# Optimization experiments

Measured on AMD Instinct MI355X. Metric: run time of the kernel, lower is better.

Reference implementation:

```python
import jax, jax.numpy as jnp
import numpy as np

GS, SO = 5, 3  # KANLinear grid_size, spline_order (efficient-kan defaults)


def kan_linear(x, base_w, spline_w, spline_scaler):
    """efficient-kan KANLinear: silu(x)@Wb^T + Bspline(x) contracted with scaled spline weights."""
    g = jnp.arange(-SO, GS + SO + 1, dtype=x.dtype) * (2.0 / GS) - 1.0  # uniform grid, len 12
    xe = x[..., None]                                                    # (..., in, 1)
    bases = ((xe >= g[:-1]) & (xe < g[1:])).astype(x.dtype)              # (..., in, 11)
    for k in range(1, SO + 1):  # Cox-de Boor recursion -> (..., in, 8)
        bases = ((xe - g[:-(k + 1)]) / (g[k:-1] - g[:-(k + 1)])) * bases[..., :-1] \
              + ((g[k + 1:] - xe) / (g[k + 1:] - g[1:-k])) * bases[..., 1:]
    out = jax.nn.silu(x) @ base_w.T
    return out + jnp.einsum('...ik,oik->...o', bases, spline_w * spline_scaler[..., None])


def reference(hidden_states, in_bw, in_sw, in_sc, conv_w, conv_b, x_bw, x_sw, x_sc,
              dt_w, dt_bias, A_logs, Ds, out_bw, out_sw, out_sc):
    B, N, L, Dm = hidden_states.shape
    d_inner, _, d_conv = conv_w.shape
    K = dt_bias.shape[0]          # 4 scan directions
    d_state = A_logs.shape[1]
    dt_rank = dt_w.shape[1]

    xz = kan_linear(hidden_states, in_bw, in_sw, in_sc)          # (B,N,L,2*Di)
    x, z = jnp.split(xz, 2, axis=-1)

    # causal depthwise conv1d + SiLU (torch pads both sides then truncates to L == left-pad)
    xc = x.reshape(B * N, L, d_inner).transpose(0, 2, 1)          # (BN,Di,L)
    xc = jax.lax.conv_general_dilated(xc, conv_w, (1,), [(d_conv - 1, 0)],
                                      dimension_numbers=('NCH', 'OIH', 'NCH'),
                                      feature_group_count=d_inner)
    xc = jax.nn.silu(xc + conv_b[None, :, None])
    x = xc.transpose(0, 2, 1).reshape(B, N, L, d_inner)

    xs = jnp.concatenate([x, jnp.flip(x, axis=2)], axis=1)        # (B,4,L,Di): fwd + seq-reversed

    x_dbl = kan_linear(xs, x_bw, x_sw, x_sc)                      # (B,4,L,R+2S)
    dt, Bs, Cs = jnp.split(x_dbl, [dt_rank, dt_rank + d_state], axis=-1)
    dts = dt @ dt_w.T                                             # (B,4,L,Di)
    delta = jax.nn.softplus(dts + dt_bias[None, :, None, :])      # (B,4,L,Di)
    A = -jnp.exp(A_logs).reshape(K, d_inner, d_state)             # (4,Di,S)

    # selective scan over L (serial data-dependent linear recurrence)
    u_t = xs.transpose(2, 0, 1, 3)      # (L,B,4,Di)
    d_t = delta.transpose(2, 0, 1, 3)   # (L,B,4,Di)
    B_t = Bs.transpose(2, 0, 1, 3)      # (L,B,4,S)
    C_t = Cs.transpose(2, 0, 1, 3)      # (L,B,4,S)

    def step(h, inp):
        u_l, dl, b_l, c_l = inp
        h = h * jnp.exp(dl[..., None] * A) + (dl * u_l)[..., None] * b_l[:, :, None, :]
        return h, jnp.einsum('bkdn,bkn->bkd', h, c_l)

    h0 = jnp.zeros((B, K, d_inner, d_state), xs.dtype)
    _, ys = jax.lax.scan(step, h0, (u_t, d_t, B_t, C_t))          # ys: (L,B,4,Di)

    y = ys.transpose(1, 2, 0, 3) + xs * Ds.reshape(K, d_inner)[None, :, None, :]  # (B,4,L,Di)
    y = y[:, :2] + jnp.flip(y[:, 2:4], axis=2)                    # merge forward/backward scans

    out = jnp.concatenate([y, z], axis=-1)                        # (B,2,L,2*Di)
    return kan_linear(out, out_bw, out_sw, out_sc)                # (B,2,L,Dm)


def setup_inputs() -> dict:
    key = jax.random.key(0)
    B, N, L = 2, 2, 1024
    d_model, d_state, d_conv, K = 512, 16, 4, 4
    d_inner = d_model            # expand=1
    dt_rank = 32                 # ceil(512/16)
    ks = jax.random.split(key, 10)

    def lin(k, o, i):
        return jax.random.normal(k, (o, i), jnp.float32) / np.sqrt(i).astype(np.float32)

    def spl(k, o, i):
        return jax.random.normal(k, (o, i, GS + SO), jnp.float32) * 0.05

    dt = jnp.exp(jax.random.uniform(ks[7], (d_inner,), jnp.float32)
                 * (np.log(0.1) - np.log(0.001)) + np.log(0.001))
    dt = jnp.clip(dt, 1e-4, None)
    inv_dt = dt + jnp.log(-jnp.expm1(-dt))

    std = dt_rank ** -0.5
    return {
        'hidden_states': jax.random.normal(ks[0], (B, N, L, d_model), jnp.float32),
        'in_bw': lin(ks[1], 2 * d_inner, d_model),
        'in_sw': spl(ks[2], 2 * d_inner, d_model),
        'in_sc': jnp.ones((2 * d_inner, d_model), jnp.float32),
        'conv_w': jax.random.normal(ks[3], (d_inner, 1, d_conv), jnp.float32) / np.sqrt(d_conv).astype(np.float32),
        'conv_b': jnp.zeros((d_inner,), jnp.float32),
        'x_bw': lin(ks[4], dt_rank + 2 * d_state, d_inner),
        'x_sw': spl(ks[5], dt_rank + 2 * d_state, d_inner),
        'x_sc': jnp.ones((dt_rank + 2 * d_state, d_inner), jnp.float32),
        'dt_w': jax.random.uniform(ks[6], (d_inner, dt_rank), jnp.float32, -std, std),
        'dt_bias': jnp.tile(inv_dt[None], (K, 1)),
        'A_logs': jnp.log(jnp.tile(jnp.arange(1, d_state + 1, dtype=jnp.float32)[None], (K * d_inner, 1))),
        'Ds': jnp.ones((K * d_inner,), jnp.float32),
        'out_bw': lin(ks[8], d_model, 2 * d_inner),
        'out_sw': spl(ks[9], d_model, 2 * d_inner),
        'out_sc': jnp.ones((d_model, 2 * d_inner), jnp.float32),
    }
```

## Files before the change

### kernel.cpp

```cpp
#include <hip/hip_runtime.h>
#include <stdint.h>

#define DEV __device__ __forceinline__

typedef __attribute__((ext_vector_type(8))) short short8;
typedef __attribute__((ext_vector_type(4))) float f32x4;

DEV unsigned short f2bf(float f) {
    union { float f; uint32_t u; } v; v.f = f;
    uint32_t u = v.u;
    return (unsigned short)((u + 0x7fffu + ((u >> 16) & 1u)) >> 16);
}
DEV float silu_f(float x) { return x / (1.0f + __expf(-x)); }
DEV float softplus_f(float x) { return (x > 20.0f) ? x : log1pf(__expf(x)); }

DEV int tokx(int bk, int l) {
    int b = bk >> 2;
    int nn = bk & 1;
    int lf = (bk & 2) ? (1023 - l) : l;
    return (b * 2 + nn) * 1024 + lf;
}

DEV void bspline8(float x, float* bo) {
    float b[11];
#pragma unroll
    for (int j = 0; j < 11; ++j) {
        float gj  = 0.4f * (float)(j - 3) - 1.0f;
        float gj1 = 0.4f * (float)(j - 2) - 1.0f;
        b[j] = (x >= gj && x < gj1) ? 1.0f : 0.0f;
    }
#pragma unroll
    for (int k = 1; k <= 3; ++k) {
        float inv = 1.0f / (0.4f * (float)k);
#pragma unroll
        for (int j = 0; j + k < 11; ++j) {
            float gj  = 0.4f * (float)(j - 3) - 1.0f;
            float gk1 = 0.4f * (float)(j + k - 2) - 1.0f;
            b[j] = ((x - gj) * b[j] + (gk1 - x) * b[j + 1]) * inv;
        }
    }
#pragma unroll
    for (int j = 0; j < 8; ++j) bo[j] = b[j];
}

__global__ __launch_bounds__(256) void zero_kernel(float4* __restrict__ p, int n4) {
    int i = blockIdx.x * 256 + threadIdx.x;
    if (i < n4) p[i] = make_float4(0.f, 0.f, 0.f, 0.f);
}

__global__ __launch_bounds__(256) void add3_kernel(float4* __restrict__ dst,
        const float4* __restrict__ s1, const float4* __restrict__ s2, int n4) {
    int i = blockIdx.x * 256 + threadIdx.x;
    if (i >= n4) return;
    float4 d = dst[i], a = s1[i], b = s2[i];
    d.x += a.x + b.x; d.y += a.y + b.y; d.z += a.z + b.z; d.w += a.w + b.w;
    dst[i] = d;
}

__global__ __launch_bounds__(256) void wcFM_kernel(const float* __restrict__ bw,
        const float* __restrict__ sw, const float* __restrict__ sc,
        unsigned short* __restrict__ Wc, int OUT, int IN) {
    int gid = blockIdx.x * 256 + threadIdx.x;
    int perRow = IN >> 3;
    if (gid >= OUT * perRow) return;
    int o  = gid / perRow;
    int i0 = (gid % perRow) * 8;
    const float* bwp = bw + (size_t)o * IN + i0;
    const float* scp = sc + (size_t)o * IN + i0;
    const float* swp = sw + ((size_t)o * IN + i0) * 8;
    float bwv[8], scv[8], swv[64];
    *(float4*)&bwv[0] = *(const float4*)bwp;
    *(float4*)&bwv[4] = *(const float4*)(bwp + 4);
    *(float4*)&scv[0] = *(const float4*)scp;
    *(float4*)&scv[4] = *(const float4*)(scp + 4);
#pragma unroll
    for (int q = 0; q < 16; ++q) *(float4*)&swv[q * 4] = *(const float4*)(swp + q * 4);
    unsigned short* row = Wc + (size_t)o * 9 * IN + i0;
    short8 v;
#pragma unroll
    for (int e = 0; e < 8; ++e) v[e] = f2bf(bwv[e]);
    *(short8*)row = v;
#pragma unroll
    for (int j = 1; j <= 8; ++j) {
#pragma unroll
        for (int e = 0; e < 8; ++e) v[e] = f2bf(swv[e * 8 + (j - 1)] * scv[e]);
        *(short8*)&row[(size_t)j * IN] = v;
    }
}

__global__ __launch_bounds__(256) void featFM_kernel(const float* __restrict__ X,
        unsigned short* __restrict__ F, int ntok, int IN) {
    int gid = blockIdx.x * 256 + threadIdx.x;
    int perRow = IN >> 3;
    if (gid >= ntok * perRow) return;
    int t  = gid / perRow;
    int i0 = (gid % perRow) * 8;
    const float* xp = X + (size_t)t * IN + i0;
    float xv[8];
    *(float4*)&xv[0] = *(const float4*)xp;
    *(float4*)&xv[4] = *(const float4*)(xp + 4);
    float bases[8][8];
    short8 v;
#pragma unroll
    for (int e = 0; e < 8; ++e) {
        v[e] = f2bf(silu_f(xv[e]));
        bspline8(xv[e], bases[e]);
    }
    unsigned short* row = F + (size_t)t * 9 * IN + i0;
    *(short8*)row = v;
#pragma unroll
    for (int j = 1; j <= 8; ++j) {
#pragma unroll
        for (int e = 0; e < 8; ++e) v[e] = f2bf(bases[e][j - 1]);
        *(short8*)&row[(size_t)j * IN] = v;
    }
}

template<int BM, int BN, int DEPTH, bool ATOMIC>
__global__ __launch_bounds__(256) void gemm_mfma2(const unsigned short* __restrict__ A,
        const unsigned short* __restrict__ B, float* __restrict__ C0,
        float* __restrict__ C1, float* __restrict__ C2,
        int M, int N, int K, int klen, int gx, int gy, int gz) {
    constexpr int NB  = DEPTH + 2;
    constexpr int FRM = BM / 32;
    constexpr int FRN = BN / 32;
    constexpr int GLA = (BM * 64) / 4096;
    constexpr int GLB = (BN * 64) / 4096;
    constexpr int GL  = GLA + GLB;
    constexpr int LDA = BM * 32;
    constexpr int LDB = BN * 32;
    __shared__ unsigned short As[NB * LDA];
    __shared__ unsigned short Bs[NB * LDB];

    const int nwg = gx * gy * gz;
    int fid = (blockIdx.z * gy + blockIdx.y) * gx + blockIdx.x;
    int cpx = nwg >> 3;
    fid = (fid & 7) * cpx + (fid >> 3);
    const int by = fid % gy;
    const int bx = (fid / gy) % gx;
    const int bz = fid / (gy * gx);

    const int tid = threadIdx.x;
    const int lane = tid & 63;
    const int w = tid >> 6;
    const int wr = w >> 1, wc = w & 1;
    const int bm = bx * BM, bn = by * BN;
    const int kbase = bz * klen;
    const int NT = klen / 32;
    const int frow = lane & 15;
    const int uq = ((lane >> 4) ^ ((frow >> 1) & 3)) * 8;

    float* __restrict__ C = (bz == 0) ? C0 : (bz == 1) ? C1 : C2;

    f32x4 acc[FRM][FRN];
#pragma unroll
    for (int m = 0; m < FRM; ++m)
#pragma unroll
        for (int n = 0; n < FRN; ++n)
            acc[m][n] = (f32x4){0.f, 0.f, 0.f, 0.f};

    auto stage = [&](int t, int buf) {
        const int k0 = kbase + t * 32;
#pragma unroll
        for (int r = 0; r < GLA; ++r) {
            int bo = r * 4096 + tid * 16;
            int row = bo >> 6;
            int lu = ((bo >> 4) & 3) ^ ((row >> 1) & 3);
            __builtin_amdgcn_global_load_lds(
                (const __attribute__((address_space(1))) void*)((const char*)A + ((size_t)(bm + row) * K + k0) * 2 + lu * 16),
                (__attribute__((address_space(3))) void*)((char*)As + (size_t)buf * LDA * 2 + bo), 16, 0, 0);
        }
#pragma unroll
        for (int r = 0; r < GLB; ++r) {
            int bo = r * 4096 + tid * 16;
            int row = bo >> 6;
            int lu = ((bo >> 4) & 3) ^ ((row >> 1) & 3);
            __builtin_amdgcn_global_load_lds(
                (const __attribute__((address_space(1))) void*)((const char*)B + ((size_t)(bn + row) * K + k0) * 2 + lu * 16),
                (__attribute__((address_space(3))) void*)((char*)Bs + (size_t)buf * LDB * 2 + bo), 16, 0, 0);
        }
    };

    auto compute = [&](int buf) {
        const unsigned short* as = As + (size_t)buf * LDA;
        const unsigned short* bs = Bs + (size_t)buf * LDB;
        short8 af[FRM], bf[FRN];
#pragma unroll
        for (int m = 0; m < FRM; ++m)
            af[m] = *(const short8*)&as[(wr * (BM / 2) + m * 16 + frow) * 32 + uq];
#pragma unroll
        for (int n = 0; n < FRN; ++n)
            bf[n] = *(const short8*)&bs[(wc * (BN / 2) + n * 16 + frow) * 32 + uq];
#pragma unroll
        for (int m = 0; m < FRM; ++m)
#pragma unroll
            for (int n = 0; n < FRN; ++n)
                acc[m][n] = __builtin_amdgcn_mfma_f32_16x16x32_bf16(af[m], bf[n], acc[m][n], 0, 0, 0);
    };

    for (int t = 0; t < DEPTH; ++t) stage(t, t);

    int rb = 0, sb = DEPTH;
    int t = 0;
    for (; t + DEPTH < NT; ++t) {
        stage(t + DEPTH, sb);
        asm volatile("s_waitcnt vmcnt(%0)" :: "i"(DEPTH * GL) : "memory");
        asm volatile("s_barrier" ::: "memory");
        compute(rb);
        rb = (rb + 1 == NB) ? 0 : rb + 1;
        sb = (sb + 1 == NB) ? 0 : sb + 1;
    }
    for (; t < NT; ++t) {
        asm volatile("s_waitcnt vmcnt(0)" ::: "memory");
        asm volatile("s_barrier" ::: "memory");
        compute(rb);
        rb = (rb + 1 == NB) ? 0 : rb + 1;
    }

    const int crow = (lane >> 4) * 4;
    const int ccol = lane & 15;
#pragma unroll
    for (int m = 0; m < FRM; ++m)
#pragma unroll
        for (int n = 0; n < FRN; ++n) {
            int gr = bm + wr * (BM / 2) + m * 16 + crow;
            int gc = bn + wc * (BN / 2) + n * 16 + ccol;
#pragma unroll
            for (int r = 0; r < 4; ++r) {
                if (ATOMIC) atomicAdd(&C[(size_t)(gr + r) * N + gc], acc[m][n][r]);
                else        C[(size_t)(gr + r) * N + gc] = acc[m][n][r];
            }
        }
}

__global__ __launch_bounds__(256) void conv_xs_kernel(const float* __restrict__ xz,
        const float* __restrict__ cw, const float* __restrict__ cb,
        float* __restrict__ xsb) {
    int idx = blockIdx.x * 256 + threadIdx.x;
    int d = idx & 511;
    int l = (idx >> 9) & 1023;
    int bn = idx >> 19;
    const float* xcol = xz + (size_t)(bn * 1024) * 1024 + d;
    float acc = cb[d];
#pragma unroll
    for (int h = 0; h < 4; ++h) {
        int ls = l - 3 + h;
        float xv = (ls >= 0) ? xcol[(size_t)ls * 1024] : 0.0f;
        acc = fmaf(cw[d * 4 + h], xv, acc);
    }
    xsb[((size_t)bn * 1024 + l) * 512 + d] = silu_f(acc);
}

__global__ __launch_bounds__(256) void dts_kernel(const float* __restrict__ xdbl,
        const float* __restrict__ dtw, float* __restrict__ dts) {
    int t = blockIdx.x >> 1;
    int half = blockIdx.x & 1;
    int d = half * 256 + threadIdx.x;
    __shared__ float dtv[32];
    if (threadIdx.x < 32) dtv[threadIdx.x] = xdbl[(size_t)t * 64 + threadIdx.x];
    __syncthreads();
    const float* w = dtw + (size_t)d * 32;
    float acc = 0.0f;
#pragma unroll
    for (int r = 0; r < 32; r += 4) {
        float4 wv = *(const float4*)(w + r);
        acc = fmaf(dtv[r], wv.x, acc);
        acc = fmaf(dtv[r + 1], wv.y, acc);
        acc = fmaf(dtv[r + 2], wv.z, acc);
        acc = fmaf(dtv[r + 3], wv.w, acc);
    }
    dts[(size_t)t * 512 + d] = acc;
}

__global__ __launch_bounds__(256) void scanA_kernel(const float* __restrict__ dts,
        const float* __restrict__ xsb, const float* __restrict__ xdbl,
        const float* __restrict__ A_logs, const float* __restrict__ dtb,
        float* __restrict__ P, float* __restrict__ Q) {
    int half = blockIdx.x & 1;
    int chunk = (blockIdx.x >> 1) & 31;
    int bk = blockIdx.x >> 6;
    int k = bk & 3;
    int d = half * 256 + threadIdx.x;
    __shared__ float Bl[32][16];
    for (int s = threadIdx.x; s < 32 * 16; s += 256) {
        int ll = s >> 4, n = s & 15;
        Bl[ll][n] = xdbl[(size_t)tokx(bk, chunk * 32 + ll) * 64 + 32 + n];
    }
    __syncthreads();
    float An[16];
#pragma unroll
    for (int n = 0; n < 16; ++n) An[n] = -__expf(A_logs[(size_t)(k * 512 + d) * 16 + n]);
    float bias = dtb[k * 512 + d];
    float h[16] = {};
    float p[16];
#pragma unroll
    for (int n = 0; n < 16; ++n) p[n] = 1.0f;
    for (int ll = 0; ll < 32; ++ll) {
        size_t off = (size_t)tokx(bk, chunk * 32 + ll) * 512 + d;
        float da = softplus_f(dts[off] + bias);
        float du = da * xsb[off];
#pragma unroll
        for (int n = 0; n < 16; ++n) {
            float a = __expf(da * An[n]);
            h[n] = fmaf(h[n], a, du * Bl[ll][n]);
            p[n] *= a;
        }
    }
    size_t pb = ((size_t)(bk * 32 + chunk) * 16) * 512 + d;
#pragma unroll
    for (int n = 0; n < 16; ++n) { P[pb + n * 512] = p[n]; Q[pb + n * 512] = h[n]; }
}

__global__ __launch_bounds__(512) void scanB_kernel(const float* __restrict__ P,
        const float* __restrict__ Q, float* __restrict__ Hst) {
    int bk = blockIdx.x >> 4;
    int n  = blockIdx.x & 15;
    int d  = threadIdx.x;
    float h = 0.0f;
    for (int chunk = 0; chunk < 32; ++chunk) {
        size_t base = ((size_t)((bk * 32 + chunk) * 16 + n)) * 512 + d;
        Hst[base] = h;
        h = fmaf(P[base], h, Q[base]);
    }
}

__global__ __launch_bounds__(256) void scanC_kernel(const float* __restrict__ dts,
        const float* __restrict__ xsb, const float* __restrict__ xdbl,
        const float* __restrict__ A_logs, const float* __restrict__ dtb,
        const float* __restrict__ Hst, const float* __restrict__ Ds,
        float* __restrict__ ys) {
    int half = blockIdx.x & 1;
    int chunk = (blockIdx.x >> 1) & 31;
    int bk = blockIdx.x >> 6;
    int k = bk & 3;
    int d = half * 256 + threadIdx.x;
    __shared__ float BC[32][32];
    for (int s = threadIdx.x; s < 32 * 32; s += 256) {
        int ll = s >> 5, n = s & 31;
        BC[ll][n] = xdbl[(size_t)tokx(bk, chunk * 32 + ll) * 64 + 32 + n];
    }
    __syncthreads();
    float An[16];
#pragma unroll
    for (int n = 0; n < 16; ++n) An[n] = -__expf(A_logs[(size_t)(k * 512 + d) * 16 + n]);
    float bias = dtb[k * 512 + d];
    float h[16];
    size_t hb = ((size_t)(bk * 32 + chunk) * 16) * 512 + d;
#pragma unroll
    for (int n = 0; n < 16; ++n) h[n] = Hst[hb + n * 512];
    float Dv = Ds[k * 512 + d];
    for (int ll = 0; ll < 32; ++ll) {
        int l = chunk * 32 + ll;
        size_t off = (size_t)tokx(bk, l) * 512 + d;
        float da = softplus_f(dts[off] + bias);
        float u = xsb[off];
        float du = da * u;
        float y = 0.0f;
#pragma unroll
        for (int n = 0; n < 16; ++n) {
            float a = __expf(da * An[n]);
            h[n] = fmaf(h[n], a, du * BC[ll][n]);
            y = fmaf(h[n], BC[ll][16 + n], y);
        }
        ys[((size_t)bk * 1024 + l) * 512 + d] = fmaf(u, Dv, y);
    }
}

__global__ __launch_bounds__(256) void merge_kernel(const float* __restrict__ ys,
        float* __restrict__ xz) {
    int idx = blockIdx.x * 256 + threadIdx.x;
    int d = idx & 511;
    int l = (idx >> 9) & 1023;
    int nn = (idx >> 19) & 1;
    int b = idx >> 20;
    float v = ys[((size_t)(b * 4 + nn) * 1024 + l) * 512 + d]
            + ys[((size_t)(b * 4 + nn + 2) * 1024 + (1023 - l)) * 512 + d];
    size_t trow = (size_t)(b * 2 + nn) * 1024 + l;
    xz[trow * 1024 + d] = v;
}

extern "C" void kernel_launch(void* const* d_in, const int* in_sizes, int n_in,
                              void* d_out, int out_size, void* d_ws, size_t ws_size,
                              hipStream_t stream) {
    const float* hidden  = (const float*)d_in[0];
    const float* in_bw   = (const float*)d_in[1];
    const float* in_sw   = (const float*)d_in[2];
    const float* in_sc   = (const float*)d_in[3];
    const float* conv_w  = (const float*)d_in[4];
    const float* conv_b  = (const float*)d_in[5];
    const float* x_bw    = (const float*)d_in[6];
    const float* x_sw    = (const float*)d_in[7];
    const float* x_sc    = (const float*)d_in[8];
    const float* dt_w    = (const float*)d_in[9];
    const float* dt_bias = (const float*)d_in[10];
    const float* A_logs  = (const float*)d_in[11];
    const float* Ds      = (const float*)d_in[12];
    const float* out_bw  = (const float*)d_in[13];
    const float* out_sw  = (const float*)d_in[14];
    const float* out_sc  = (const float*)d_in[15];
    float* out = (float*)d_out;
    char* ws = (char*)d_ws;

    float* XZ    = (float*)(ws + 0);
    float* XSB   = (float*)(ws + 16777216);
    float* XDBL  = (float*)(ws + 25165824);
    float* DTS   = (float*)(ws + 26214400);
    char*  zone  = ws + 34603008;
    unsigned short* FEAT = (unsigned short*)zone;
    float* YS    = (float*)zone;
    float* P     = (float*)(zone + 16777216);
    float* Q     = (float*)(zone + 25165824);
    float* HST   = (float*)(zone + 33554432);
    float* XZP1  = (float*)(zone + 37748736);
    float* XZP2  = (float*)(zone + 54525952);
    float* OP1   = (float*)(ws + 16777216);
    float* OP2   = (float*)(ws + 26214400);
    unsigned short* WCbuf = (unsigned short*)(ws + 110100480);
    unsigned short* WC2   = (unsigned short*)(ws + 119537664);

    wcFM_kernel<<<256, 256, 0, stream>>>(in_bw, in_sw, in_sc, WCbuf, 1024, 512);
    wcFM_kernel<<<16, 256, 0, stream>>>(x_bw, x_sw, x_sc, WC2, 64, 512);

    featFM_kernel<<<1024, 256, 0, stream>>>(hidden, FEAT, 4096, 512);
    gemm_mfma2<128, 128, 1, false><<<dim3(32, 8, 3), 256, 0, stream>>>(
        FEAT, WCbuf, XZ, XZP1, XZP2, 4096, 1024, 4608, 1536, 32, 8, 3);
    add3_kernel<<<4096, 256, 0, stream>>>((float4*)XZ, (const float4*)XZP1, (const float4*)XZP2, (4096 * 1024) / 4);

    wcFM_kernel<<<256, 256, 0, stream>>>(out_bw, out_sw, out_sc, WCbuf, 512, 1024);

    conv_xs_kernel<<<8192, 256, 0, stream>>>(XZ, conv_w, conv_b, XSB);

    featFM_kernel<<<1024, 256, 0, stream>>>(XSB, FEAT, 4096, 512);
    zero_kernel<<<256, 256, 0, stream>>>((float4*)XDBL, (4096 * 64) / 4);
    gemm_mfma2<64, 64, 1, true><<<dim3(64, 1, 8), 256, 0, stream>>>(
        FEAT, WC2, XDBL, XDBL, XDBL, 4096, 64, 4608, 576, 64, 1, 8);

    dts_kernel<<<8192, 256, 0, stream>>>(XDBL, dt_w, DTS);

    scanA_kernel<<<512, 256, 0, stream>>>(DTS, XSB, XDBL, A_logs, dt_bias, P, Q);
    scanB_kernel<<<128, 512, 0, stream>>>(P, Q, HST);
    scanC_kernel<<<512, 256, 0, stream>>>(DTS, XSB, XDBL, A_logs, dt_bias, HST, Ds, YS);

    merge_kernel<<<8192, 256, 0, stream>>>(YS, XZ);

    featFM_kernel<<<2048, 256, 0, stream>>>(XZ, FEAT, 4096, 1024);
    gemm_mfma2<128, 64, 1, false><<<dim3(32, 8, 3), 256, 0, stream>>>(
        FEAT, WCbuf, out, OP1, OP2, 4096, 512, 9216, 3072, 32, 8, 3);
    add3_kernel<<<2048, 256, 0, stream>>>((float4*)out, (const float4*)OP1,
        (const float4*)OP2, (4096 * 512) / 4);
}
```

Measured before the change: 441.0 us.

## Fuse conv into feature build and use atomic split-K instead of partial buffers

The depthwise causal conv + SiLU is merged with the KAN feature expansion (silu + B-spline bases to bf16) into one kernel. That kernel writes XSB and the feature matrix directly, which removes a separate pass that re-read XSB. The split-K GEMMs for in_proj and out_proj now accumulate with atomicAdd into a memset-zeroed output, instead of writing three partial buffers and summing them with an add3 kernel. This cuts memory traffic and kernel launches, at the cost of float atomics, which make the summation order nondeterministic.

Measured after the change: 473.4 us. +7.3%, slower.

```diff
diff --git a/kernel.cpp b/kernel.cpp
--- a/kernel.cpp
+++ b/kernel.cpp
@@ -41,20 +41,6 @@
     }
 #pragma unroll
     for (int j = 0; j < 8; ++j) bo[j] = b[j];
-}
-
-__global__ __launch_bounds__(256) void zero_kernel(float4* __restrict__ p, int n4) {
-    int i = blockIdx.x * 256 + threadIdx.x;
-    if (i < n4) p[i] = make_float4(0.f, 0.f, 0.f, 0.f);
-}
-
-__global__ __launch_bounds__(256) void add3_kernel(float4* __restrict__ dst,
-        const float4* __restrict__ s1, const float4* __restrict__ s2, int n4) {
-    int i = blockIdx.x * 256 + threadIdx.x;
-    if (i >= n4) return;
-    float4 d = dst[i], a = s1[i], b = s2[i];
-    d.x += a.x + b.x; d.y += a.y + b.y; d.z += a.z + b.z; d.w += a.w + b.w;
-    dst[i] = d;
 }
 
 __global__ __launch_bounds__(256) void wcFM_kernel(const float* __restrict__ bw,
@@ -116,10 +102,52 @@
     }
 }
 
-template<int BM, int BN, int DEPTH, bool ATOMIC>
+__global__ __launch_bounds__(256) void conv_feat_kernel(const float* __restrict__ xz,
+        const float* __restrict__ cw, const float* __restrict__ cb,
+        float* __restrict__ xsb, unsigned short* __restrict__ F) {
+    int gid = blockIdx.x * 256 + threadIdx.x;
+    int tk = gid >> 6;
+    int i0 = (gid & 63) * 8;
+    int l  = tk & 1023;
+    const float* base = xz + (size_t)(tk - l) * 1024 + i0;
+    float acc[8];
+#pragma unroll
+    for (int e = 0; e < 8; ++e) acc[e] = cb[i0 + e];
+#pragma unroll
+    for (int h = 0; h < 4; ++h) {
+        int ls = l - 3 + h;
+        if (ls >= 0) {
+            float xv[8];
+            *(float4*)&xv[0] = *(const float4*)(base + (size_t)ls * 1024);
+            *(float4*)&xv[4] = *(const float4*)(base + (size_t)ls * 1024 + 4);
+#pragma unroll
+            for (int e = 0; e < 8; ++e) acc[e] = fmaf(cw[(i0 + e) * 4 + h], xv[e], acc[e]);
+        }
+    }
+    float v8[8];
+    float bases[8][8];
+    short8 v;
+#pragma unroll
+    for (int e = 0; e < 8; ++e) {
+        v8[e] = silu_f(acc[e]);
+        v[e] = f2bf(silu_f(v8[e]));
+        bspline8(v8[e], bases[e]);
+    }
+    *(float4*)&xsb[(size_t)tk * 512 + i0]     = *(float4*)&v8[0];
+    *(float4*)&xsb[(size_t)tk * 512 + i0 + 4] = *(float4*)&v8[4];
+    unsigned short* row = F + (size_t)tk * 4608 + i0;
+    *(short8*)row = v;
+#pragma unroll
+    for (int j = 1; j <= 8; ++j) {
+#pragma unroll
+        for (int e = 0; e < 8; ++e) v[e] = f2bf(bases[e][j - 1]);
+        *(short8*)&row[(size_t)j * 512] = v;
+    }
+}
+
+template<int BM, int BN, int DEPTH>
 __global__ __launch_bounds__(256) void gemm_mfma2(const unsigned short* __restrict__ A,
-        const unsigned short* __restrict__ B, float* __restrict__ C0,
-        float* __restrict__ C1, float* __restrict__ C2,
+        const unsigned short* __restrict__ B, float* __restrict__ C,
         int M, int N, int K, int klen, int gx, int gy, int gz) {
     constexpr int NB  = DEPTH + 2;
     constexpr int FRM = BM / 32;
@@ -150,8 +178,6 @@
     const int frow = lane & 15;
     const int uq = ((lane >> 4) ^ ((frow >> 1) & 3)) * 8;
 
-    float* __restrict__ C = (bz == 0) ? C0 : (bz == 1) ? C1 : C2;
-
     f32x4 acc[FRM][FRN];
 #pragma unroll
     for (int m = 0; m < FRM; ++m)
@@ -226,29 +252,9 @@
             int gr = bm + wr * (BM / 2) + m * 16 + crow;
             int gc = bn + wc * (BN / 2) + n * 16 + ccol;
 #pragma unroll
-            for (int r = 0; r < 4; ++r) {
-                if (ATOMIC) atomicAdd(&C[(size_t)(gr + r) * N + gc], acc[m][n][r]);
-                else        C[(size_t)(gr + r) * N + gc] = acc[m][n][r];
-            }
-        }
-}
-
-__global__ __launch_bounds__(256) void conv_xs_kernel(const float* __restrict__ xz,
-        const float* __restrict__ cw, const float* __restrict__ cb,
-        float* __restrict__ xsb) {
-    int idx = blockIdx.x * 256 + threadIdx.x;
-    int d = idx & 511;
-    int l = (idx >> 9) & 1023;
-    int bn = idx >> 19;
-    const float* xcol = xz + (size_t)(bn * 1024) * 1024 + d;
-    float acc = cb[d];
-#pragma unroll
-    for (int h = 0; h < 4; ++h) {
-        int ls = l - 3 + h;
-        float xv = (ls >= 0) ? xcol[(size_t)ls * 1024] : 0.0f;
-        acc = fmaf(cw[d * 4 + h], xv, acc);
-    }
-    xsb[((size_t)bn * 1024 + l) * 512 + d] = silu_f(acc);
+            for (int r = 0; r < 4; ++r)
+                atomicAdd(&C[(size_t)(gr + r) * N + gc], acc[m][n][r]);
+        }
 }
 
 __global__ __launch_bounds__(256) void dts_kernel(const float* __restrict__ xdbl,
@@ -411,10 +417,6 @@
     float* P     = (float*)(zone + 16777216);
     float* Q     = (float*)(zone + 25165824);
     float* HST   = (float*)(zone + 33554432);
-    float* XZP1  = (float*)(zone + 37748736);
-    float* XZP2  = (float*)(zone + 54525952);
-    float* OP1   = (float*)(ws + 16777216);
-    float* OP2   = (float*)(ws + 26214400);
     unsigned short* WCbuf = (unsigned short*)(ws + 110100480);
     unsigned short* WC2   = (unsigned short*)(ws + 119537664);
 
@@ -422,18 +424,17 @@
     wcFM_kernel<<<16, 256, 0, stream>>>(x_bw, x_sw, x_sc, WC2, 64, 512);
 
     featFM_kernel<<<1024, 256, 0, stream>>>(hidden, FEAT, 4096, 512);
-    gemm_mfma2<128, 128, 1, false><<<dim3(32, 8, 3), 256, 0, stream>>>(
-        FEAT, WCbuf, XZ, XZP1, XZP2, 4096, 1024, 4608, 1536, 32, 8, 3);
-    add3_kernel<<<4096, 256, 0, stream>>>((float4*)XZ, (const float4*)XZP1, (const float4*)XZP2, (4096 * 1024) / 4);
+    hipMemsetAsync(XZ, 0, (size_t)4096 * 1024 * 4, stream);
+    gemm_mfma2<128, 128, 1><<<dim3(32, 8, 3), 256, 0, stream>>>(
+        FEAT, WCbuf, XZ, 4096, 1024, 4608, 1536, 32, 8, 3);
 
     wcFM_kernel<<<256, 256, 0, stream>>>(out_bw, out_sw, out_sc, WCbuf, 512, 1024);
 
-    conv_xs_kernel<<<8192, 256, 0, stream>>>(XZ, conv_w, conv_b, XSB);
-
-    featFM_kernel<<<1024, 256, 0, stream>>>(XSB, FEAT, 4096, 512);
-    zero_kernel<<<256, 256, 0, stream>>>((float4*)XDBL, (4096 * 64) / 4);
-    gemm_mfma2<64, 64, 1, true><<<dim3(64, 1, 8), 256, 0, stream>>>(
-        FEAT, WC2, XDBL, XDBL, XDBL, 4096, 64, 4608, 576, 64, 1, 8);
+    conv_feat_kernel<<<1024, 256, 0, stream>>>(XZ, conv_w, conv_b, XSB, FEAT);
+
+    hipMemsetAsync(XDBL, 0, (size_t)4096 * 64 * 4, stream);
+    gemm_mfma2<64, 64, 1><<<dim3(64, 1, 8), 256, 0, stream>>>(
+        FEAT, WC2, XDBL, 4096, 64, 4608, 576, 64, 1, 8);
 
     dts_kernel<<<8192, 256, 0, stream>>>(XDBL, dt_w, DTS);
 
@@ -444,8 +445,7 @@
     merge_kernel<<<8192, 256, 0, stream>>>(YS, XZ);
 
     featFM_kernel<<<2048, 256, 0, stream>>>(XZ, FEAT, 4096, 1024);
-    gemm_mfma2<128, 64, 1, false><<<dim3(32, 8, 3), 256, 0, stream>>>(
-        FEAT, WCbuf, out, OP1, OP2, 4096, 512, 9216, 3072, 32, 8, 3);
-    add3_kernel<<<2048, 256, 0, stream>>>((float4*)out, (const float4*)OP1,
-        (const float4*)OP2, (4096 * 512) / 4);
-}
+    hipMemsetAsync(out, 0, (size_t)4096 * 512 * 4, stream);
+    gemm_mfma2<128, 64, 1><<<dim3(32, 8, 3), 256, 0, stream>>>(
+        FEAT, WCbuf, out, 4096, 512, 9216, 3072, 32, 8, 3);
+}
```
